# Kernel optimization log

Measured on AMD Instinct MI355X. Metric: run time of the kernel, lower is better.

Reference implementation:

```python
import jax, jax.numpy as jnp
import numpy as np

BITS = 12
BATCH = 4194304

# Boolean algebra on {0,1}-valued floats (matches spiking XOR/AND/OR gate logic)
def _xor(x, y):
    return x + y - 2.0 * x * y

def _and(x, y):
    return x * y

def _or(x, y):
    return x + y - x * y


def setup_inputs() -> dict:
    key = jax.random.key(0)
    kA, kB = jax.random.split(key)
    A = jax.random.randint(kA, (BATCH, BITS), 0, 2).astype(jnp.float32)
    B = jax.random.randint(kB, (BATCH, BITS), 0, 2).astype(jnp.float32)
    return {"A": A, "B": B}


def reference(A, B):
    """12-bit ripple-carry adder. Bit index 11 is the LSB (loop runs 11->0).
    Returns (sum_bits [..., 12], carry_out [..., 1])."""
    def step(carry, ab):
        a, b = ab  # each [batch...]
        t1 = _xor(a, b)
        s = _xor(t1, carry)
        new_carry = _or(_or(_and(a, b), _and(a, carry)), _and(b, carry))
        return new_carry, s

    # scan from LSB (index 11) to MSB (index 0): reverse bit axis, move to front
    xs = (jnp.moveaxis(A[..., ::-1], -1, 0), jnp.moveaxis(B[..., ::-1], -1, 0))  # [12, batch]
    carry0 = jnp.zeros(A.shape[:-1], A.dtype)
    carry, sums = jax.lax.scan(step, carry0, xs)
    sums = jnp.moveaxis(sums, 0, -1)[..., ::-1]  # back to [..., 12], MSB-first
    return sums, carry[..., None]
```

## Files before the change

kernel.cpp:

```cpp
#include <hip/hip_runtime.h>


#define BATCH 4194304
#define BITS  12

__global__ __launch_bounds__(256) void adder12_kernel(
    const uint4* __restrict__ A,
    const uint4* __restrict__ B,
    uint4* __restrict__ sums,
    unsigned* __restrict__ carry)
{
    const unsigned ONE = 0x3F800000u;
    const long long stride = (long long)gridDim.x * blockDim.x;
    for (long long i = (long long)blockIdx.x * blockDim.x + threadIdx.x;
         i < BATCH; i += stride) {

        const uint4* a4 = A + i * 3;
        const uint4* b4 = B + i * 3;
        uint4 av0 = a4[0], av1 = a4[1], av2 = a4[2];
        uint4 bv0 = b4[0], bv1 = b4[1], bv2 = b4[2];

        unsigned au[12] = {av0.x, av0.y, av0.z, av0.w,
                           av1.x, av1.y, av1.z, av1.w,
                           av2.x, av2.y, av2.z, av2.w};
        unsigned bu[12] = {bv0.x, bv0.y, bv0.z, bv0.w,
                           bv1.x, bv1.y, bv1.z, bv1.w,
                           bv2.x, bv2.y, bv2.z, bv2.w};

        unsigned ua = 0u, ub = 0u;
        #pragma unroll
        for (int j = 0; j < 12; ++j) {
            ua |= ((au[j] >> 29) & 1u) << (11 - j);
            ub |= ((bu[j] >> 29) & 1u) << (11 - j);
        }

        const unsigned s = ua + ub;

        unsigned of[12];
        #pragma unroll
        for (int j = 0; j < 12; ++j)
            of[j] = ((s >> (11 - j)) & 1u) ? ONE : 0u;

        uint4* o4 = sums + i * 3;
        o4[0] = make_uint4(of[0],  of[1],  of[2],  of[3]);
        o4[1] = make_uint4(of[4],  of[5],  of[6],  of[7]);
        o4[2] = make_uint4(of[8],  of[9],  of[10], of[11]);

        carry[i] = ((s >> 12) & 1u) ? ONE : 0u;
    }
}

extern "C" void kernel_launch(void* const* d_in, const int* in_sizes, int n_in,
                              void* d_out, int out_size, void* d_ws, size_t ws_size,
                              hipStream_t stream) {
    const uint4* A = (const uint4*)d_in[0];
    const uint4* B = (const uint4*)d_in[1];
    uint4* sums     = (uint4*)d_out;
    unsigned* carry = (unsigned*)d_out + (size_t)BATCH * 12;

    dim3 grid(2048), block(256);
    adder12_kernel<<<grid, block, 0, stream>>>(A, B, sums, carry);
}
```

Measured before the change: 467.3 us.

## Process two rows per thread with fixed unrolled loop and nontemporal stores

Each thread now handles two adjacent rows per iteration over a compile-time trip count, fully unrolled, so more independent loads are in flight per thread. Outputs are written with nontemporal stores to reduce cache pollution, and the carry is written as a two-element vector. The kernel is hard-wired to the grid and batch sizes, and each thread's accesses become wider-strided, which may hurt coalescing.

```diff
diff --git a/kernel.cpp b/kernel.cpp
--- a/kernel.cpp
+++ b/kernel.cpp
@@ -1,63 +1,79 @@
 #include <hip/hip_runtime.h>
 
 
-#define BATCH 4194304
-#define BITS  12
+typedef unsigned uv4 __attribute__((ext_vector_type(4)));
+typedef unsigned uv2 __attribute__((ext_vector_type(2)));
+
+#define BATCHN  4194304u
+#define NBLOCKS 2048u
+#define NTH     (NBLOCKS * 256u)
+#define ITERS   (BATCHN / (NTH * 2u))
 
 __global__ __launch_bounds__(256) void adder12_kernel(
-    const uint4* __restrict__ A,
-    const uint4* __restrict__ B,
-    uint4* __restrict__ sums,
-    unsigned* __restrict__ carry)
+    const uv4* __restrict__ A4,
+    const uv4* __restrict__ B4,
+    uv4* __restrict__ S4,
+    uv2* __restrict__ C2)
 {
     const unsigned ONE = 0x3F800000u;
-    const long long stride = (long long)gridDim.x * blockDim.x;
-    for (long long i = (long long)blockIdx.x * blockDim.x + threadIdx.x;
-         i < BATCH; i += stride) {
+    const unsigned gid = blockIdx.x * 256u + threadIdx.x;
 
-        const uint4* a4 = A + i * 3;
-        const uint4* b4 = B + i * 3;
-        uint4 av0 = a4[0], av1 = a4[1], av2 = a4[2];
-        uint4 bv0 = b4[0], bv1 = b4[1], bv2 = b4[2];
+    #pragma unroll
+    for (unsigned it = 0; it < ITERS; ++it) {
+        const size_t row0 = 2u * ((size_t)it * NTH + gid);
+        const size_t p = row0 * 3;
 
-        unsigned au[12] = {av0.x, av0.y, av0.z, av0.w,
-                           av1.x, av1.y, av1.z, av1.w,
-                           av2.x, av2.y, av2.z, av2.w};
-        unsigned bu[12] = {bv0.x, bv0.y, bv0.z, bv0.w,
-                           bv1.x, bv1.y, bv1.z, bv1.w,
-                           bv2.x, bv2.y, bv2.z, bv2.w};
+        uv4 ra0 = A4[p+0], ra1 = A4[p+1], ra2 = A4[p+2];
+        uv4 ra3 = A4[p+3], ra4 = A4[p+4], ra5 = A4[p+5];
+        uv4 rb0 = B4[p+0], rb1 = B4[p+1], rb2 = B4[p+2];
+        uv4 rb3 = B4[p+3], rb4 = B4[p+4], rb5 = B4[p+5];
 
-        unsigned ua = 0u, ub = 0u;
-        #pragma unroll
-        for (int j = 0; j < 12; ++j) {
-            ua |= ((au[j] >> 29) & 1u) << (11 - j);
-            ub |= ((bu[j] >> 29) & 1u) << (11 - j);
-        }
+        auto pack = [](uv4 v0, uv4 v1, uv4 v2) -> unsigned {
+            unsigned u[12] = {v0.x, v0.y, v0.z, v0.w,
+                              v1.x, v1.y, v1.z, v1.w,
+                              v2.x, v2.y, v2.z, v2.w};
+            unsigned r = 0u;
+            #pragma unroll
+            for (int j = 0; j < 12; ++j)
+                r |= ((u[j] >> 29) & 1u) << (11 - j);
+            return r;
+        };
 
-        const unsigned s = ua + ub;
+        const unsigned s0 = pack(ra0, ra1, ra2) + pack(rb0, rb1, rb2);
+        const unsigned s1 = pack(ra3, ra4, ra5) + pack(rb3, rb4, rb5);
 
-        unsigned of[12];
-        #pragma unroll
-        for (int j = 0; j < 12; ++j)
-            of[j] = ((s >> (11 - j)) & 1u) ? ONE : 0u;
+        auto unp = [ONE](unsigned s, int j) -> unsigned {
+            return ((s >> (11 - j)) & 1u) ? ONE : 0u;
+        };
 
-        uint4* o4 = sums + i * 3;
-        o4[0] = make_uint4(of[0],  of[1],  of[2],  of[3]);
-        o4[1] = make_uint4(of[4],  of[5],  of[6],  of[7]);
-        o4[2] = make_uint4(of[8],  of[9],  of[10], of[11]);
+        uv4 o0 = {unp(s0,0), unp(s0,1), unp(s0,2),  unp(s0,3)};
+        uv4 o1 = {unp(s0,4), unp(s0,5), unp(s0,6),  unp(s0,7)};
+        uv4 o2 = {unp(s0,8), unp(s0,9), unp(s0,10), unp(s0,11)};
+        uv4 o3 = {unp(s1,0), unp(s1,1), unp(s1,2),  unp(s1,3)};
+        uv4 o4 = {unp(s1,4), unp(s1,5), unp(s1,6),  unp(s1,7)};
+        uv4 o5 = {unp(s1,8), unp(s1,9), unp(s1,10), unp(s1,11)};
 
-        carry[i] = ((s >> 12) & 1u) ? ONE : 0u;
+        __builtin_nontemporal_store(o0, &S4[p+0]);
+        __builtin_nontemporal_store(o1, &S4[p+1]);
+        __builtin_nontemporal_store(o2, &S4[p+2]);
+        __builtin_nontemporal_store(o3, &S4[p+3]);
+        __builtin_nontemporal_store(o4, &S4[p+4]);
+        __builtin_nontemporal_store(o5, &S4[p+5]);
+
+        uv2 cv = {((s0 >> 12) & 1u) ? ONE : 0u,
+                  ((s1 >> 12) & 1u) ? ONE : 0u};
+        __builtin_nontemporal_store(cv, &C2[(size_t)it * NTH + gid]);
     }
 }
 
 extern "C" void kernel_launch(void* const* d_in, const int* in_sizes, int n_in,
                               void* d_out, int out_size, void* d_ws, size_t ws_size,
                               hipStream_t stream) {
-    const uint4* A = (const uint4*)d_in[0];
-    const uint4* B = (const uint4*)d_in[1];
-    uint4* sums     = (uint4*)d_out;
-    unsigned* carry = (unsigned*)d_out + (size_t)BATCH * 12;
+    const uv4* A = (const uv4*)d_in[0];
+    const uv4* B = (const uv4*)d_in[1];
+    uv4* sums = (uv4*)d_out;
+    uv2* c2   = (uv2*)((float*)d_out + (size_t)BATCHN * 12);
 
-    dim3 grid(2048), block(256);
-    adder12_kernel<<<grid, block, 0, stream>>>(A, B, sums, carry);
+    dim3 grid(NBLOCKS), block(256);
+    adder12_kernel<<<grid, block, 0, stream>>>(A, B, sums, c2);
 }
```

Result: slower. 787.4 us (+68.5%).
